# Optimization experiments

Measured on AMD Instinct MI355X. Metric: run time of the kernel, lower is better.

The kernel has to match this reference:

```python
import jax, jax.numpy as jnp
import numpy as np
from jax import lax

D_MODEL = 2048
D_STATE = 16
D_CONV = 4
D_INNER = 4096   # expand * d_model
DT_RANK = 128    # ceil(d_model / 16)
BATCH = 4
SEQLEN = 2048


def setup_inputs() -> dict:
    key = jax.random.key(0)
    ks = jax.random.split(key, 8)
    rnd = lambda k, shape, s: jax.random.normal(k, shape, dtype=jnp.float32) * s
    hidden_states = rnd(ks[0], (BATCH, SEQLEN, D_MODEL), 1.0)
    in_proj_w = rnd(ks[1], (2 * D_INNER, D_MODEL), D_MODEL ** -0.5)
    conv_w = rnd(ks[2], (D_INNER, 1, D_CONV), 0.3)
    conv_b = rnd(ks[3], (D_INNER,), 0.1)
    x_proj_w = rnd(ks[4], (DT_RANK + 2 * D_STATE, D_INNER), D_INNER ** -0.5)
    dt_proj_w = rnd(ks[5], (D_INNER, DT_RANK), DT_RANK ** -0.5)
    dt_proj_b = rnd(ks[6], (D_INNER,), 0.5) - 2.0  # bias dt small, like mamba dt init
    out_proj_w = rnd(ks[7], (D_MODEL, D_INNER), D_INNER ** -0.5)
    # A init: -exp(log(arange(1..N))) broadcast over channels -> (d_state, d_inner)
    A = -jnp.tile(jnp.arange(1, D_STATE + 1, dtype=jnp.float32)[:, None], (1, D_INNER))
    D = jnp.ones((D_INNER,), dtype=jnp.float32)
    conv_state = jnp.zeros((BATCH, D_INNER, D_CONV), jnp.float32)
    ssm_state = jnp.zeros((BATCH, D_STATE, D_INNER), jnp.float32)
    last_token_ids = jnp.full((BATCH,), SEQLEN, dtype=jnp.int32)
    return dict(hidden_states=hidden_states, last_token_ids=last_token_ids,
                conv_state=conv_state, ssm_state=ssm_state,
                remove_padding=False, batch_size=BATCH,
                in_proj_w=in_proj_w, conv_w=conv_w, conv_b=conv_b,
                x_proj_w=x_proj_w, dt_proj_w=dt_proj_w, dt_proj_b=dt_proj_b,
                A=A, D=D, out_proj_w=out_proj_w)


def _mamba_forward(hidden_states, in_proj_w, conv_w, conv_b, x_proj_w,
                   dt_proj_w, dt_proj_b, A, D, out_proj_w):
    b, L, _ = hidden_states.shape
    # in_proj (no bias)
    xz = jnp.einsum('bld,ed->ble', hidden_states, in_proj_w)          # (b, L, 2*d_inner)
    x, z = jnp.split(xz, 2, axis=-1)
    x_bdl = x.transpose(0, 2, 1)                                       # (b, d_inner, L)
    # present conv state = last d_conv columns of pre-conv x (F.pad with negative pad)
    new_conv_state = x_bdl[:, :, L - D_CONV:]
    # causal depthwise conv1d (left pad d_conv-1 == pad-both then truncate to L)
    x_conv = lax.conv_general_dilated(
        x_bdl, conv_w, window_strides=(1,), padding=[(D_CONV - 1, 0)],
        feature_group_count=D_INNER,
        dimension_numbers=('NCH', 'OIH', 'NCH')) + conv_b[None, :, None]
    u = jax.nn.silu(x_conv).transpose(0, 2, 1)                          # (b, L, d_inner)
    # x_proj -> dt, B, C
    x_dbl = jnp.einsum('bld,ed->ble', u, x_proj_w)
    dt, Bm, Cm = jnp.split(x_dbl, [DT_RANK, DT_RANK + D_STATE], axis=-1)
    dt = jnp.einsum('blr,dr->bld', dt, dt_proj_w)                       # no bias here
    # selective scan (delta_bias=dt_proj_b, delta_softplus=True)
    delta = jax.nn.softplus(dt + dt_proj_b)                             # (b, L, d_inner)
    dBu = delta * u                                                     # (b, L, d_inner)

    def step(x_state, inp):
        d_i, bu_i, B_i, C_i = inp                                       # (b,d),(b,d),(b,n),(b,n)
        dA = jnp.exp(d_i[:, None, :] * A[None])                         # (b, n, d)
        x_state = dA * x_state + B_i[:, :, None] * bu_i[:, None, :]
        y = jnp.einsum('bnd,bn->bd', x_state, C_i)
        return x_state, y

    x0 = jnp.zeros((b, D_STATE, D_INNER), jnp.float32)
    xs = (delta.transpose(1, 0, 2), dBu.transpose(1, 0, 2),
          Bm.transpose(1, 0, 2), Cm.transpose(1, 0, 2))
    last_state, ys = lax.scan(step, x0, xs)
    y = ys.transpose(1, 0, 2) + u * D                                   # + D skip
    y = y * jax.nn.silu(z)                                              # gate
    out = jnp.einsum('bld,ed->ble', y, out_proj_w)                      # out_proj (no bias)
    return out, new_conv_state, last_state


def reference(hidden_states, last_token_ids, conv_state, ssm_state,
              remove_padding, batch_size,
              in_proj_w, conv_w, conv_b, x_proj_w, dt_proj_w, dt_proj_b,
              A, D, out_proj_w):
    # remove_padding=False and last_token_ids all == L: the torch per-sequence
    # loop is exactly one batched forward_impl with seqlen_offset=0.
    return _mamba_forward(hidden_states, in_proj_w, conv_w, conv_b, x_proj_w,
                          dt_proj_w, dt_proj_b, A, D, out_proj_w)
```

## Files before the change

### kernel.cpp

```cpp
#include <hip/hip_runtime.h>
#include <hip/hip_bf16.h>
#include <math.h>

typedef __attribute__((ext_vector_type(4))) float fvec4;
typedef __attribute__((ext_vector_type(2))) float fvec2;
typedef __attribute__((ext_vector_type(4))) int ivec4;
typedef __attribute__((ext_vector_type(4))) unsigned short usvec4;
typedef __attribute__((ext_vector_type(8))) short bf16x8;

#define SEQ 2048
#define DMODEL 2048
#define DINNER 4096
#define DSTATE 16
#define DTRANK 128
#define NB 4
#define MROWS (NB*SEQ)
#define NCHUNK 16
#define LC (SEQ/NCHUNK)

__device__ __forceinline__ float bf2f(unsigned short h){
  union{unsigned int u; float f;} v; v.u = ((unsigned int)h)<<16; return v.f;
}
__device__ __forceinline__ unsigned short f2bf(float f){
  union{float f; unsigned int u;} v; v.f=f;
  unsigned int r = v.u + 0x7fffu + ((v.u>>16)&1u);
  return (unsigned short)(r>>16);
}
__device__ __forceinline__ void async16(const void* g, void* l){
  __builtin_amdgcn_global_load_lds((const __attribute__((address_space(1))) void*)g,
                                   (__attribute__((address_space(3))) void*)l, 16, 0, 0);
}
__device__ __forceinline__ float sigf(float x){ return 1.f/(1.f+__expf(-x)); }

__global__ void cvt_bf16_kernel(const float* __restrict__ in, unsigned short* __restrict__ out, int n){
  int i = (blockIdx.x*256 + threadIdx.x)*4;
  if (i >= n) return;
  fvec4 v = *(const fvec4*)(in + i);
  usvec4 o;
  o[0]=f2bf(v[0]); o[1]=f2bf(v[1]); o[2]=f2bf(v[2]); o[3]=f2bf(v[3]);
  *(usvec4*)(out + i) = o;
}

template<int MODE>
__global__ __launch_bounds__(512, 2) void gemm256(
    const unsigned short* __restrict__ A,
    const unsigned short* __restrict__ B,
    int K, int nbx, int ldc,
    unsigned short* __restrict__ Cb1,
    unsigned short* __restrict__ Cb2,
    float* __restrict__ Cf)
{
  __shared__ __align__(16) unsigned short lds[65536];
  char* ldsc = (char*)lds;
  const int t = threadIdx.x;

  const int nwg = gridDim.x;
  const int cpx = nwg >> 3;
  const int bid = blockIdx.x;
  const int swzb = (bid & 7)*cpx + (bid >> 3);
  const int bx = swzb % nbx, by = swzb / nbx;

  const int bA0 = t*16, bA1 = 8192 + t*16;
  const int sw0 = bA0 ^ (((bA0>>7)&3)<<4);
  const int sw1 = bA1 ^ (((bA1>>7)&3)<<4);
  const int gr0 = sw0>>6, gc0 = (sw0&63)>>1;
  const int gr1 = sw1>>6, gc1 = (sw1&63)>>1;
  const unsigned short* Ab = A + (long)by*256*K;
  const unsigned short* Bb = B + (long)bx*256*K;
  const unsigned short* gA0 = Ab + (long)gr0*K + gc0;
  const unsigned short* gA1 = Ab + (long)gr1*K + gc1;
  const unsigned short* gB0 = Bb + (long)gr0*K + gc0;
  const unsigned short* gB1 = Bb + (long)gr1*K + gc1;

  const int wid = t>>6, lane = t&63;
  const int wm = wid>>2, wn = wid&3;
  const int fr = lane&15, fc = lane>>4;
  const int cb = (fc<<4) ^ (((fr>>1)&3)<<4);
  const int offA = (wm*128 + fr)*64 + cb;
  const int offB = 16384 + (wn*64 + fr)*64 + cb;

  fvec4 acc[8][4];
  #pragma unroll
  for (int i=0;i<8;i++){
    #pragma unroll
    for (int j=0;j<4;j++) acc[i][j] = (fvec4)(0.f);
  }

  const int NKT = K >> 5;
  auto stage = [&](int slot, int k0){
    char* sb = ldsc + slot*32768;
    async16(gA0 + k0, sb + t*16);
    async16(gA1 + k0, sb + 8192 + t*16);
    async16(gB0 + k0, sb + 16384 + t*16);
    async16(gB1 + k0, sb + 24576 + t*16);
  };

  stage(0, 0); stage(1, 32); stage(2, 64);

  for (int kt = 0; kt < NKT; ++kt){
    asm volatile("s_waitcnt vmcnt(8)" ::: "memory");
    __builtin_amdgcn_s_barrier();
    __builtin_amdgcn_sched_barrier(0);
    { int ks = kt + 3; if (ks > NKT-1) ks = NKT-1;
      stage((kt+3)&3, ks*32); }
    __builtin_amdgcn_sched_barrier(0);
    const char* sb = ldsc + (kt&3)*32768;
    bf16x8 af[8], bv[4];
    #pragma unroll
    for (int j=0;j<4;j++) bv[j] = *(const bf16x8*)(sb + offB + j*1024);
    #pragma unroll
    for (int i=0;i<8;i++) af[i] = *(const bf16x8*)(sb + offA + i*1024);
    __builtin_amdgcn_s_setprio(1);
    #pragma unroll
    for (int i=0;i<8;i++){
      #pragma unroll
      for (int j=0;j<4;j++){
        acc[i][j] = __builtin_amdgcn_mfma_f32_16x16x32_bf16(af[i], bv[j], acc[i][j], 0,0,0);
      }
    }
    __builtin_amdgcn_s_setprio(0);
  }

  const long crow0 = (long)by*256 + wm*128;
  const int  ccol0 = bx*256 + wn*64;
  #pragma unroll
  for (int i=0;i<8;i++){
    #pragma unroll
    for (int j=0;j<4;j++){
      #pragma unroll
      for (int q=0;q<4;q++){
        long rg = crow0 + i*16 + fc*4 + q;
        int  cg = ccol0 + j*16 + fr;
        float v = acc[i][j][q];
        if (MODE==0){
          if (cg < DINNER) Cb1[rg*DINNER + cg] = f2bf(v);
          else             Cb2[rg*DINNER + (cg-DINNER)] = f2bf(v);
        } else {
          Cf[rg*(long)ldc + cg] = v;
        }
      }
    }
  }
}

template<int MODE>
__global__ __launch_bounds__(256) void gemm_bt(
    const unsigned short* __restrict__ A,
    const unsigned short* __restrict__ B,
    int K, int Nreal,
    float* __restrict__ Cf,
    unsigned short* __restrict__ Cb1,
    const float* __restrict__ bias,
    int ldc)
{
  __shared__ __align__(16) unsigned short As[128*32];
  __shared__ __align__(16) unsigned short Bs[128*32];
  const int t = threadIdx.x;
  const int bx = blockIdx.x, by = blockIdx.y;
  const int wave = t>>6, lane = t&63;
  const int wr = (wave>>1)*64, wc = (wave&1)*64;
  const int fr = lane&15, fc = lane>>4;
  fvec4 acc[4][4];
  #pragma unroll
  for(int i=0;i<4;i++){
    #pragma unroll
    for(int j=0;j<4;j++){ acc[i][j] = (fvec4)(0.f); }
  }
  const int srow = t>>2;
  const int scol = (t&3)*8;
  long rowA = (long)by*128 + srow;
  int rB0 = bx*128 + srow;      if (rB0 > Nreal-1) rB0 = Nreal-1;
  int rB1 = bx*128 + 64 + srow; if (rB1 > Nreal-1) rB1 = Nreal-1;
  const unsigned short* gA0 = A + rowA*(long)K + scol;
  const unsigned short* gA1 = gA0 + 64L*K;
  const unsigned short* gB0 = B + (long)rB0*K + scol;
  const unsigned short* gB1 = B + (long)rB1*K + scol;
  unsigned short* lA0 = &As[t*8];
  unsigned short* lA1 = &As[2048 + t*8];
  unsigned short* lB0 = &Bs[t*8];
  unsigned short* lB1 = &Bs[2048 + t*8];

  for (int k0 = 0; k0 < K; k0 += 32){
    async16(gA0 + k0, lA0);
    async16(gA1 + k0, lA1);
    async16(gB0 + k0, lB0);
    async16(gB1 + k0, lB1);
    __syncthreads();
    bf16x8 af[4], bv[4];
    #pragma unroll
    for(int i=0;i<4;i++){
      af[i] = *(const bf16x8*)&As[(wr + i*16 + fr)*32 + fc*8];
      bv[i] = *(const bf16x8*)&Bs[(wc + i*16 + fr)*32 + fc*8];
    }
    #pragma unroll
    for(int i=0;i<4;i++){
      #pragma unroll
      for(int j=0;j<4;j++){
        acc[i][j] = __builtin_amdgcn_mfma_f32_16x16x32_bf16(af[i], bv[j], acc[i][j], 0,0,0);
      }
    }
    __syncthreads();
  }

  const long crow0 = (long)by*128 + wr;
  const int ccol0 = bx*128 + wc;
  #pragma unroll
  for(int i=0;i<4;i++){
    #pragma unroll
    for(int j=0;j<4;j++){
      #pragma unroll
      for(int q=0;q<4;q++){
        long rg = crow0 + i*16 + fc*4 + q;
        int  cg = ccol0 + j*16 + fr;
        float v = acc[i][j][q];
        if (MODE==1){
          if (cg < Nreal) Cf[rg*ldc + cg] = v;
        } else if (MODE==2){
          float x = v + bias[cg];
          float sp = (x > 20.f) ? x : log1pf(__expf(x));
          Cb1[rg*ldc + cg] = f2bf(sp);
        }
      }
    }
  }
}

__global__ __launch_bounds__(256) void conv_silu_kernel(
    const unsigned short* __restrict__ xb, const float* __restrict__ w,
    const float* __restrict__ bias, unsigned short* __restrict__ ub)
{
  int gid = blockIdx.x*256 + threadIdx.x;
  int d0 = (gid & 511)*8;
  long m = gid >> 9;
  int l = (int)(m & (SEQ-1));
  fvec4 w4[8];
  #pragma unroll
  for(int k=0;k<8;k++) w4[k] = *(const fvec4*)&w[(d0+k)*4];
  float acc[8];
  fvec4 b0 = *(const fvec4*)&bias[d0];
  fvec4 b1 = *(const fvec4*)&bias[d0+4];
  acc[0]=b0[0];acc[1]=b0[1];acc[2]=b0[2];acc[3]=b0[3];
  acc[4]=b1[0];acc[5]=b1[1];acc[6]=b1[2];acc[7]=b1[3];
  #pragma unroll
  for(int j=0;j<4;j++){
    int lj = l-3+j;
    if (lj >= 0){
      ivec4 xv = *(const ivec4*)&xb[(m-3+j)*DINNER + d0];
      float xs[8];
      #pragma unroll
      for(int q=0;q<4;q++){
        unsigned int wd = (unsigned int)xv[q];
        xs[2*q]   = bf2f((unsigned short)(wd & 0xffffu));
        xs[2*q+1] = bf2f((unsigned short)(wd >> 16));
      }
      #pragma unroll
      for(int k=0;k<8;k++) acc[k] += xs[k]*w4[k][j];
    }
  }
  ivec4 ov;
  #pragma unroll
  for(int q=0;q<4;q++){
    float y0 = acc[2*q]  * sigf(acc[2*q]);
    float y1 = acc[2*q+1]* sigf(acc[2*q+1]);
    ov[q] = (int)((unsigned)f2bf(y0) | ((unsigned)f2bf(y1) << 16));
  }
  *(ivec4*)&ub[m*DINNER + d0] = ov;
}

__global__ void conv_state_kernel(const unsigned short* __restrict__ xb, float* __restrict__ out){
  int i = blockIdx.x*256 + threadIdx.x;
  int b = i >> 14; int r = i & 16383; int dd = r >> 2; int j = r & 3;
  out[i] = bf2f(xb[((long)(b*SEQ + (SEQ-4) + j))*DINNER + dd]);
}

__global__ void cvt_dtr_kernel(const float* __restrict__ xdbl, unsigned short* __restrict__ dtr){
  int i = blockIdx.x*256 + threadIdx.x;
  long mrow = i >> 5; int c = (i & 31)*4;
  fvec4 v = *(const fvec4*)&xdbl[mrow*160 + c];
  usvec4 o; o[0]=f2bf(v[0]); o[1]=f2bf(v[1]); o[2]=f2bf(v[2]); o[3]=f2bf(v[3]);
  *(usvec4*)&dtr[mrow*DTRANK + c] = o;
}

__device__ __forceinline__ void exp_powers(float dl, float* e){
  float e1 = __expf(-dl);
  float p2 = e1*e1, p3 = p2*e1, p4 = p2*p2;
  float p5 = p4*e1, p6 = p4*p2, p7 = p4*p3, p8 = p4*p4;
  e[0]=e1; e[1]=p2; e[2]=p3; e[3]=p4; e[4]=p5; e[5]=p6; e[6]=p7; e[7]=p8;
  e[8]=p8*e1; e[9]=p8*p2; e[10]=p8*p3; e[11]=p8*p4;
  e[12]=p8*p5; e[13]=p8*p6; e[14]=p8*p7; e[15]=p8*p8;
}

__global__ __launch_bounds__(256) void scan_part1(
    const unsigned short* __restrict__ delta_b,
    const unsigned short* __restrict__ u_b,
    const float* __restrict__ xdbl,
    const float* __restrict__ Amat,
    float* __restrict__ S,
    float* __restrict__ sdelta)
{
  const int t = threadIdx.x;
  const int blk = blockIdx.x;
  const int c = blk & 15, b = (blk>>4)&3, d = (blk>>6)*256 + t;
  float a[16], s[16];
  #pragma unroll
  for (int n=0;n<16;n++){ a[n] = Amat[n*DINNER+d]; s[n]=0.f; }
  bool powA = true;
  #pragma unroll
  for (int n=0;n<16;n++) powA = powA && (a[n] == -(float)(n+1));
  float sd = 0.f;
  const long mbase = (long)b*SEQ + c*LC;

#define S1_BODY(EXPR_E) \
  for (int l=0;l<LC;l++){ \
    long m = mbase + l; \
    float dl = bf2f(delta_b[m*DINNER+d]); \
    float ul = bf2f(u_b[m*DINNER+d]); \
    const float* xb = &xdbl[m*160 + 128]; \
    float dbu = dl*ul; \
    sd += dl; \
    float e[16]; EXPR_E; \
    _Pragma("unroll") \
    for (int g=0; g<4; g++){ \
      fvec4 Bg = *(const fvec4*)(xb + 4*g); \
      _Pragma("unroll") \
      for (int q=0;q<4;q++){ \
        int n = g*4+q; \
        s[n] = e[n]*s[n] + Bg[q]*dbu; \
      } \
    } \
  }

  if (powA){
    S1_BODY(exp_powers(dl, e))
  } else {
    S1_BODY({ _Pragma("unroll") for (int n=0;n<16;n++) e[n] = __expf(dl*a[n]); })
  }
#undef S1_BODY

  const long base = ((long)(b*NCHUNK + c)*DSTATE)*DINNER + d;
  #pragma unroll
  for (int n=0;n<16;n++) S[base + (long)n*DINNER] = s[n];
  sdelta[(long)(b*NCHUNK+c)*DINNER + d] = sd;
}

__global__ __launch_bounds__(256) void scan_part2(
    const float* __restrict__ S,
    const float* __restrict__ sdelta,
    const float* __restrict__ Amat,
    float* __restrict__ Xin,
    float* __restrict__ last_state)
{
  int id = blockIdx.x*256 + threadIdx.x;
  int d = id & (DINNER-1);
  int n = (id>>12) & 15;
  int b = id>>16;
  float a = Amat[n*DINNER+d];
  float X = 0.f;
  #pragma unroll
  for (int c=0;c<NCHUNK;c++){
    long sb = ((long)(b*NCHUNK+c)*DSTATE + n)*DINNER + d;
    Xin[sb] = X;
    float sd = sdelta[(long)(b*NCHUNK+c)*DINNER + d];
    float Sc = S[sb];
    X = __expf(a*sd)*X + Sc;
  }
  last_state[((long)b*DSTATE + n)*DINNER + d] = X;
}

__global__ __launch_bounds__(256) void scan_part3(
    const unsigned short* __restrict__ delta_b,
    const unsigned short* __restrict__ u_b,
    const unsigned short* __restrict__ z_b,
    const float* __restrict__ xdbl,
    const float* __restrict__ Amat,
    const float* __restrict__ Dvec,
    const float* __restrict__ Xin,
    unsigned short* __restrict__ y_b)
{
  const int t = threadIdx.x;
  const int blk = blockIdx.x;
  const int c = blk & 15, b = (blk>>4)&3, d = (blk>>6)*256 + t;
  float a[16], s[16];
  const long xb0 = ((long)(b*NCHUNK + c)*DSTATE)*DINNER + d;
  #pragma unroll
  for (int n=0;n<16;n++){
    a[n] = Amat[n*DINNER+d];
    s[n] = Xin[xb0 + (long)n*DINNER];
  }
  bool powA = true;
  #pragma unroll
  for (int n=0;n<16;n++) powA = powA && (a[n] == -(float)(n+1));
  const float Dd = Dvec[d];
  const long mbase = (long)b*SEQ + c*LC;

#define S3_BODY(EXPR_E) \
  for (int l=0;l<LC;l++){ \
    long m = mbase + l; \
    float dl = bf2f(delta_b[m*DINNER+d]); \
    float ul = bf2f(u_b[m*DINNER+d]); \
    float zl = bf2f(z_b[m*DINNER+d]); \
    const float* xb = &xdbl[m*160 + 128]; \
    float dbu = dl*ul; \
    float y = 0.f; \
    float e[16]; EXPR_E; \
    _Pragma("unroll") \
    for (int g=0; g<4; g++){ \
      fvec4 Bg = *(const fvec4*)(xb + 4*g); \
      fvec4 Cg = *(const fvec4*)(xb + 16 + 4*g); \
      _Pragma("unroll") \
      for (int q=0;q<4;q++){ \
        int n = g*4+q; \
        s[n] = e[n]*s[n] + Bg[q]*dbu; \
        y += Cg[q]*s[n]; \
      } \
    } \
    float yy = y + ul*Dd; \
    float zs = zl*sigf(zl); \
    y_b[m*DINNER+d] = f2bf(yy*zs); \
  }

  if (powA){
    S3_BODY(exp_powers(dl, e))
  } else {
    S3_BODY({ _Pragma("unroll") for (int n=0;n<16;n++) e[n] = __expf(dl*a[n]); })
  }
#undef S3_BODY
}

extern "C" void kernel_launch(void* const* d_in, const int* in_sizes, int n_in,
                              void* d_out, int out_size, void* d_ws, size_t ws_size,
                              hipStream_t stream) {
  const float* hs     = (const float*)d_in[0];
  const float* w_in   = (const float*)d_in[6];
  const float* conv_w = (const float*)d_in[7];
  const float* conv_b = (const float*)d_in[8];
  const float* w_xp   = (const float*)d_in[9];
  const float* w_dt   = (const float*)d_in[10];
  const float* dt_bias= (const float*)d_in[11];
  const float* Amat   = (const float*)d_in[12];
  const float* Dvec   = (const float*)d_in[13];
  const float* w_out  = (const float*)d_in[14];
  float* out = (float*)d_out;

  char* ws = (char*)d_ws;
  const size_t MiB = (size_t)1 << 20;

  unsigned short *hs_b, *w_in_b, *x_b, *z_b, *u_b, *delta_b;
  unsigned short *wxp_b, *wdt_b, *wout_b, *dtr_b, *y_b;
  float *xdbl, *Sbuf, *Xin, *sdelta;

  if (ws_size >= 400*MiB){
    size_t off = 0;
    auto alloc = [&](size_t bytes)->void*{ void* p = ws + off; off += (bytes + 255) & ~(size_t)255; return p; };
    hs_b   = (unsigned short*)alloc((size_t)MROWS*DMODEL*2);
    w_in_b = (unsigned short*)alloc((size_t)2*DINNER*DMODEL*2);
    x_b    = (unsigned short*)alloc((size_t)MROWS*DINNER*2);
    z_b    = (unsigned short*)alloc((size_t)MROWS*DINNER*2);
    u_b    = (unsigned short*)alloc((size_t)MROWS*DINNER*2);
    delta_b= (unsigned short*)alloc((size_t)MROWS*DINNER*2);
    wxp_b  = (unsigned short*)alloc((size_t)160*DINNER*2);
    wdt_b  = (unsigned short*)alloc((size_t)DINNER*DTRANK*2);
    wout_b = (unsigned short*)alloc((size_t)DMODEL*DINNER*2);
    xdbl   = (float*)alloc((size_t)MROWS*160*4);
    dtr_b  = (unsigned short*)alloc((size_t)MROWS*DTRANK*2);
    Sbuf   = (float*)alloc((size_t)NB*NCHUNK*DSTATE*DINNER*4);
    Xin    = (float*)alloc((size_t)NB*NCHUNK*DSTATE*DINNER*4);
    sdelta = (float*)alloc((size_t)NB*NCHUNK*DINNER*4);
    y_b    = x_b;
  } else {
    hs_b    = (unsigned short*)(ws + 0);
    w_in_b  = (unsigned short*)(ws + 32*MiB);
    delta_b = (unsigned short*)(ws + 0);
    x_b     = (unsigned short*)(ws + 64*MiB);
    wxp_b   = (unsigned short*)(ws + 64*MiB);
    wdt_b   = (unsigned short*)(ws + 66*MiB);
    wout_b  = (unsigned short*)(ws + 68*MiB);
    xdbl    = (float*)         (ws + 84*MiB);
    dtr_b   = (unsigned short*)(ws + 90*MiB);
    Sbuf    = (float*)         (ws + 92*MiB);
    Xin     = (float*)         (ws + 108*MiB);
    sdelta  = (float*)         (ws + 124*MiB);
    z_b     = (unsigned short*)(ws + 128*MiB);
    u_b     = (unsigned short*)(ws + 192*MiB);
    y_b     = u_b;
  }

  cvt_bf16_kernel<<<(MROWS*DMODEL)/1024, 256, 0, stream>>>(hs, hs_b, MROWS*DMODEL);
  cvt_bf16_kernel<<<(2*DINNER*DMODEL)/1024, 256, 0, stream>>>(w_in, w_in_b, 2*DINNER*DMODEL);

  gemm256<0><<<1024, 512, 0, stream>>>(hs_b, w_in_b, DMODEL, 32, 0,
                                       x_b, z_b, nullptr);
  conv_state_kernel<<<256, 256, 0, stream>>>(x_b, out + (size_t)MROWS*DMODEL);
  conv_silu_kernel<<<(MROWS*512)/256, 256, 0, stream>>>(x_b, conv_w, conv_b, u_b);

  cvt_bf16_kernel<<<(160*DINNER)/1024, 256, 0, stream>>>(w_xp, wxp_b, 160*DINNER);
  cvt_bf16_kernel<<<(DINNER*DTRANK)/1024, 256, 0, stream>>>(w_dt, wdt_b, DINNER*DTRANK);
  cvt_bf16_kernel<<<(DMODEL*DINNER)/1024, 256, 0, stream>>>(w_out, wout_b, DMODEL*DINNER);

  gemm_bt<1><<<dim3(2,64), 256, 0, stream>>>(u_b, wxp_b, DINNER, 160,
                                             xdbl, nullptr, nullptr, 160);
  cvt_dtr_kernel<<<(MROWS*32)/256, 256, 0, stream>>>(xdbl, dtr_b);
  gemm_bt<2><<<dim3(32,64), 256, 0, stream>>>(dtr_b, wdt_b, DTRANK, DINNER,
                                              nullptr, delta_b, dt_bias, DINNER);
  scan_part1<<<1024, 256, 0, stream>>>(delta_b, u_b, xdbl, Amat, Sbuf, sdelta);
  scan_part2<<<1024, 256, 0, stream>>>(Sbuf, sdelta, Amat, Xin,
                                       out + (size_t)MROWS*DMODEL + NB*DINNER*4);
  scan_part3<<<1024, 256, 0, stream>>>(delta_b, u_b, z_b, xdbl, Amat, Dvec, Xin, y_b);
  gemm256<3><<<256, 512, 0, stream>>>(y_b, wout_b, DINNER, 8, DMODEL,
                                      nullptr, nullptr, out);
}
```

Measured before the change: 912.5 us.

## Rework gemm256 into BK=64 double-buffered phased pipeline; split-K x_proj GEMM

The main 256x256 GEMM now loads 64-wide K tiles into two 64KB LDS buffers with a new XOR swizzle. Each K step is split into four MMA phases, and the next tile's A/B loads are interleaved between them, replacing the previous 4-slot, 32-wide ring. Separately, the skinny x_proj GEMM (only 128 blocks) is split-K four ways to raise parallelism. A new reduce kernel sums the partials and also produces the bf16 dt_rank slice, replacing cvt_dtr_kernel. The split-K adds partial-buffer traffic, and the new pipeline uses many more barriers per K step.

```diff
diff --git a/kernel.cpp b/kernel.cpp
--- a/kernel.cpp
+++ b/kernel.cpp
@@ -60,24 +60,23 @@
   const int swzb = (bid & 7)*cpx + (bid >> 3);
   const int bx = swzb % nbx, by = swzb / nbx;
 
-  const int bA0 = t*16, bA1 = 8192 + t*16;
-  const int sw0 = bA0 ^ (((bA0>>7)&3)<<4);
-  const int sw1 = bA1 ^ (((bA1>>7)&3)<<4);
-  const int gr0 = sw0>>6, gc0 = (sw0&63)>>1;
-  const int gr1 = sw1>>6, gc1 = (sw1&63)>>1;
-  const unsigned short* Ab = A + (long)by*256*K;
-  const unsigned short* Bb = B + (long)bx*256*K;
-  const unsigned short* gA0 = Ab + (long)gr0*K + gc0;
-  const unsigned short* gA1 = Ab + (long)gr1*K + gc1;
-  const unsigned short* gB0 = Bb + (long)gr0*K + gc0;
-  const unsigned short* gB1 = Bb + (long)gr1*K + gc1;
-
   const int wid = t>>6, lane = t&63;
   const int wm = wid>>2, wn = wid&3;
   const int fr = lane&15, fc = lane>>4;
-  const int cb = (fc<<4) ^ (((fr>>1)&3)<<4);
-  const int offA = (wm*128 + fr)*64 + cb;
-  const int offB = 16384 + (wn*64 + fr)*64 + cb;
+  const int x0 = ((fc ^ (fr&7))<<4);
+  const int x1 = (((4+fc) ^ (fr&7))<<4);
+  const int arowB = (wm*128 + fr)*128;
+  const int browB = 32768 + (wn*64 + fr)*128;
+
+  const int r0 = t>>3;
+  const int cel = ((((t&7) ^ (r0&7))<<4))>>1;
+  const unsigned short* Ab = A + (long)by*256*K;
+  const unsigned short* Bb = B + (long)bx*256*K;
+  const unsigned short* gA0 = Ab + (long)r0*K + cel;
+  const unsigned short* gA1 = Ab + (long)(128+r0)*K + cel;
+  const unsigned short* gB0 = Bb + (long)r0*K + cel;
+  const unsigned short* gB1 = Bb + (long)(128+r0)*K + cel;
+  const int dL0 = t*16, dL1 = 8192 + t*16;
 
   fvec4 acc[8][4];
   #pragma unroll
@@ -86,40 +85,72 @@
     for (int j=0;j<4;j++) acc[i][j] = (fvec4)(0.f);
   }
 
-  const int NKT = K >> 5;
-  auto stage = [&](int slot, int k0){
-    char* sb = ldsc + slot*32768;
-    async16(gA0 + k0, sb + t*16);
-    async16(gA1 + k0, sb + 8192 + t*16);
-    async16(gB0 + k0, sb + 16384 + t*16);
-    async16(gB1 + k0, sb + 24576 + t*16);
-  };
-
-  stage(0, 0); stage(1, 32); stage(2, 64);
+  const int NKT = K >> 6;
+  const long K64 = 64L*K;
+
+#define STAGE_A(nb_, k0_) { \
+    async16(gA0 + (k0_), (nb_) + dL0); async16(gA0 + (k0_) + K64, (nb_) + dL1); \
+    async16(gA1 + (k0_), (nb_) + 16384 + dL0); async16(gA1 + (k0_) + K64, (nb_) + 16384 + dL1); }
+#define STAGE_B(nb_, k0_) { \
+    async16(gB0 + (k0_), (nb_) + 32768 + dL0); async16(gB0 + (k0_) + K64, (nb_) + 32768 + dL1); \
+    async16(gB1 + (k0_), (nb_) + 49152 + dL0); async16(gB1 + (k0_) + K64, (nb_) + 49152 + dL1); }
+
+  bf16x8 af[8], bv[4];
+#define RD_A(IH) { _Pragma("unroll") for (int i=0;i<4;i++){ \
+    const char* p_ = db + arowB + (IH)*8192 + i*2048; \
+    af[i*2]   = *(const bf16x8*)(p_ + x0); \
+    af[i*2+1] = *(const bf16x8*)(p_ + x1); }}
+#define RD_B(JH) { _Pragma("unroll") for (int j=0;j<2;j++){ \
+    const char* p_ = db + browB + (JH)*4096 + j*2048; \
+    bv[j*2]   = *(const bf16x8*)(p_ + x0); \
+    bv[j*2+1] = *(const bf16x8*)(p_ + x1); }}
+#define BARR { __builtin_amdgcn_s_barrier(); __builtin_amdgcn_sched_barrier(0); }
+#define LGKM0 { asm volatile("s_waitcnt lgkmcnt(0)" ::: "memory"); __builtin_amdgcn_sched_barrier(0); }
+#define PH_MMA(IB, JB) { \
+    __builtin_amdgcn_s_setprio(1); \
+    _Pragma("unroll") for (int i=0;i<4;i++){ \
+      _Pragma("unroll") for (int j=0;j<2;j++){ \
+        acc[(IB)+i][(JB)+j] = __builtin_amdgcn_mfma_f32_16x16x32_bf16(af[i*2],   bv[j*2],   acc[(IB)+i][(JB)+j], 0,0,0); \
+        acc[(IB)+i][(JB)+j] = __builtin_amdgcn_mfma_f32_16x16x32_bf16(af[i*2+1], bv[j*2+1], acc[(IB)+i][(JB)+j], 0,0,0); \
+      }} \
+    __builtin_amdgcn_s_setprio(0); }
+
+  STAGE_A(ldsc, 0); STAGE_B(ldsc, 0);
+  asm volatile("s_waitcnt vmcnt(0)" ::: "memory");
+  BARR;
 
   for (int kt = 0; kt < NKT; ++kt){
-    asm volatile("s_waitcnt vmcnt(8)" ::: "memory");
-    __builtin_amdgcn_s_barrier();
-    __builtin_amdgcn_sched_barrier(0);
-    { int ks = kt + 3; if (ks > NKT-1) ks = NKT-1;
-      stage((kt+3)&3, ks*32); }
-    __builtin_amdgcn_sched_barrier(0);
-    const char* sb = ldsc + (kt&3)*32768;
-    bf16x8 af[8], bv[4];
-    #pragma unroll
-    for (int j=0;j<4;j++) bv[j] = *(const bf16x8*)(sb + offB + j*1024);
-    #pragma unroll
-    for (int i=0;i<8;i++) af[i] = *(const bf16x8*)(sb + offA + i*1024);
-    __builtin_amdgcn_s_setprio(1);
-    #pragma unroll
-    for (int i=0;i<8;i++){
-      #pragma unroll
-      for (int j=0;j<4;j++){
-        acc[i][j] = __builtin_amdgcn_mfma_f32_16x16x32_bf16(af[i], bv[j], acc[i][j], 0,0,0);
-      }
-    }
-    __builtin_amdgcn_s_setprio(0);
-  }
+    const char* db = ldsc + (kt&1)*65536;
+    char* nb = ldsc + ((kt+1)&1)*65536;
+    int ks = kt + 1; if (ks > NKT-1) ks = NKT-1;
+    const int k0 = ks*64;
+    RD_A(0); RD_B(0);
+    STAGE_A(nb, k0);
+    BARR; LGKM0;
+    PH_MMA(0, 0);
+    BARR;
+    RD_B(1);
+    STAGE_B(nb, k0);
+    BARR; LGKM0;
+    PH_MMA(0, 2);
+    BARR;
+    RD_A(1);
+    BARR; LGKM0;
+    PH_MMA(4, 2);
+    BARR;
+    RD_B(0);
+    asm volatile("s_waitcnt vmcnt(0)" ::: "memory");
+    BARR; LGKM0;
+    PH_MMA(4, 0);
+    BARR;
+  }
+#undef STAGE_A
+#undef STAGE_B
+#undef RD_A
+#undef RD_B
+#undef BARR
+#undef LGKM0
+#undef PH_MMA
 
   const long crow0 = (long)by*256 + wm*128;
   const int  ccol0 = bx*256 + wn*64;
@@ -147,7 +178,7 @@
 __global__ __launch_bounds__(256) void gemm_bt(
     const unsigned short* __restrict__ A,
     const unsigned short* __restrict__ B,
-    int K, int Nreal,
+    int lda, int Kloop, int Nreal,
     float* __restrict__ Cf,
     unsigned short* __restrict__ Cb1,
     const float* __restrict__ bias,
@@ -157,6 +188,7 @@
   __shared__ __align__(16) unsigned short Bs[128*32];
   const int t = threadIdx.x;
   const int bx = blockIdx.x, by = blockIdx.y;
+  const long koff = (MODE==4) ? (long)blockIdx.z * Kloop : 0;
   const int wave = t>>6, lane = t&63;
   const int wr = (wave>>1)*64, wc = (wave&1)*64;
   const int fr = lane&15, fc = lane>>4;
@@ -171,16 +203,16 @@
   long rowA = (long)by*128 + srow;
   int rB0 = bx*128 + srow;      if (rB0 > Nreal-1) rB0 = Nreal-1;
   int rB1 = bx*128 + 64 + srow; if (rB1 > Nreal-1) rB1 = Nreal-1;
-  const unsigned short* gA0 = A + rowA*(long)K + scol;
-  const unsigned short* gA1 = gA0 + 64L*K;
-  const unsigned short* gB0 = B + (long)rB0*K + scol;
-  const unsigned short* gB1 = B + (long)rB1*K + scol;
+  const unsigned short* gA0 = A + rowA*(long)lda + scol + koff;
+  const unsigned short* gA1 = gA0 + 64L*lda;
+  const unsigned short* gB0 = B + (long)rB0*lda + scol + koff;
+  const unsigned short* gB1 = B + (long)rB1*lda + scol + koff;
   unsigned short* lA0 = &As[t*8];
   unsigned short* lA1 = &As[2048 + t*8];
   unsigned short* lB0 = &Bs[t*8];
   unsigned short* lB1 = &Bs[2048 + t*8];
 
-  for (int k0 = 0; k0 < K; k0 += 32){
+  for (int k0 = 0; k0 < Kloop; k0 += 32){
     async16(gA0 + k0, lA0);
     async16(gA1 + k0, lA1);
     async16(gB0 + k0, lB0);
@@ -204,6 +236,7 @@
 
   const long crow0 = (long)by*128 + wr;
   const int ccol0 = bx*128 + wc;
+  float* Cfz = (MODE==4) ? (Cf + (long)blockIdx.z * MROWS * ldc) : Cf;
   #pragma unroll
   for(int i=0;i<4;i++){
     #pragma unroll
@@ -213,8 +246,8 @@
         long rg = crow0 + i*16 + fc*4 + q;
         int  cg = ccol0 + j*16 + fr;
         float v = acc[i][j][q];
-        if (MODE==1){
-          if (cg < Nreal) Cf[rg*ldc + cg] = v;
+        if (MODE==4){
+          if (cg < Nreal) Cfz[rg*ldc + cg] = v;
         } else if (MODE==2){
           float x = v + bias[cg];
           float sp = (x > 20.f) ? x : log1pf(__expf(x));
@@ -222,6 +255,26 @@
         }
       }
     }
+  }
+}
+
+__global__ void reduce_xproj(const float* __restrict__ part,
+                             float* __restrict__ xdbl,
+                             unsigned short* __restrict__ dtr){
+  int i = blockIdx.x*256 + threadIdx.x;
+  long base = (long)i*4;
+  fvec4 s = *(const fvec4*)&part[base];
+  #pragma unroll
+  for (int z=1; z<4; z++){
+    fvec4 p = *(const fvec4*)&part[(long)z*MROWS*160 + base];
+    s[0]+=p[0]; s[1]+=p[1]; s[2]+=p[2]; s[3]+=p[3];
+  }
+  *(fvec4*)&xdbl[base] = s;
+  long mrow = base / 160;
+  int c = (int)(base - mrow*160);
+  if (c < DTRANK){
+    usvec4 o; o[0]=f2bf(s[0]); o[1]=f2bf(s[1]); o[2]=f2bf(s[2]); o[3]=f2bf(s[3]);
+    *(usvec4*)&dtr[mrow*DTRANK + c] = o;
   }
 }
 
@@ -271,14 +324,6 @@
   int i = blockIdx.x*256 + threadIdx.x;
   int b = i >> 14; int r = i & 16383; int dd = r >> 2; int j = r & 3;
   out[i] = bf2f(xb[((long)(b*SEQ + (SEQ-4) + j))*DINNER + dd]);
-}
-
-__global__ void cvt_dtr_kernel(const float* __restrict__ xdbl, unsigned short* __restrict__ dtr){
-  int i = blockIdx.x*256 + threadIdx.x;
-  long mrow = i >> 5; int c = (i & 31)*4;
-  fvec4 v = *(const fvec4*)&xdbl[mrow*160 + c];
-  usvec4 o; o[0]=f2bf(v[0]); o[1]=f2bf(v[1]); o[2]=f2bf(v[2]); o[3]=f2bf(v[3]);
-  *(usvec4*)&dtr[mrow*DTRANK + c] = o;
 }
 
 __device__ __forceinline__ void exp_powers(float dl, float* e){
@@ -447,9 +492,9 @@
 
   unsigned short *hs_b, *w_in_b, *x_b, *z_b, *u_b, *delta_b;
   unsigned short *wxp_b, *wdt_b, *wout_b, *dtr_b, *y_b;
-  float *xdbl, *Sbuf, *Xin, *sdelta;
-
-  if (ws_size >= 400*MiB){
+  float *xdbl, *Sbuf, *Xin, *sdelta, *xpart;
+
+  if (ws_size >= 424*MiB){
     size_t off = 0;
     auto alloc = [&](size_t bytes)->void*{ void* p = ws + off; off += (bytes + 255) & ~(size_t)255; return p; };
     hs_b   = (unsigned short*)alloc((size_t)MROWS*DMODEL*2);
@@ -466,10 +511,12 @@
     Sbuf   = (float*)alloc((size_t)NB*NCHUNK*DSTATE*DINNER*4);
     Xin    = (float*)alloc((size_t)NB*NCHUNK*DSTATE*DINNER*4);
     sdelta = (float*)alloc((size_t)NB*NCHUNK*DINNER*4);
+    xpart  = (float*)alloc((size_t)4*MROWS*160*4);
     y_b    = x_b;
   } else {
     hs_b    = (unsigned short*)(ws + 0);
     w_in_b  = (unsigned short*)(ws + 32*MiB);
+    xpart   = (float*)         (ws + 0);
     delta_b = (unsigned short*)(ws + 0);
     x_b     = (unsigned short*)(ws + 64*MiB);
     wxp_b   = (unsigned short*)(ws + 64*MiB);
@@ -497,10 +544,10 @@
   cvt_bf16_kernel<<<(DINNER*DTRANK)/1024, 256, 0, stream>>>(w_dt, wdt_b, DINNER*DTRANK);
   cvt_bf16_kernel<<<(DMODEL*DINNER)/1024, 256, 0, stream>>>(w_out, wout_b, DMODEL*DINNER);
 
-  gemm_bt<1><<<dim3(2,64), 256, 0, stream>>>(u_b, wxp_b, DINNER, 160,
-                                             xdbl, nullptr, nullptr, 160);
-  cvt_dtr_kernel<<<(MROWS*32)/256, 256, 0, stream>>>(xdbl, dtr_b);
-  gemm_bt<2><<<dim3(32,64), 256, 0, stream>>>(dtr_b, wdt_b, DTRANK, DINNER,
+  gemm_bt<4><<<dim3(2,64,4), 256, 0, stream>>>(u_b, wxp_b, DINNER, 1024, 160,
+                                               xpart, nullptr, nullptr, 160);
+  reduce_xproj<<<(MROWS*160/4)/256, 256, 0, stream>>>(xpart, xdbl, dtr_b);
+  gemm_bt<2><<<dim3(32,64), 256, 0, stream>>>(dtr_b, wdt_b, DTRANK, DTRANK, DINNER,
                                               nullptr, delta_b, dt_bias, DINNER);
   scan_part1<<<1024, 256, 0, stream>>>(delta_b, u_b, xdbl, Amat, Sbuf, sdelta);
   scan_part2<<<1024, 256, 0, stream>>>(Sbuf, sdelta, Amat, Xin,
```

New measurement: 828.1 us. -9.2%, faster.
